# Kernel optimization log

Measured on AMD Instinct MI355X. Metric: run time of the kernel, lower is better.

Reference implementation:

```python
import jax, jax.numpy as jnp
import numpy as np

N, E, DIN, H, D = 100000, 1600000, 256, 4, 32  # nodes, edges, in_feats, heads, out_feats
NEG_SLOPE = 0.2


def setup_inputs() -> dict:
    key = jax.random.key(0)
    ks = jax.random.split(key, 6)
    feat = jax.random.normal(ks[0], (N, DIN), jnp.float32)
    src = jax.random.randint(ks[1], (E,), 0, N, jnp.int32)
    dst = jax.random.randint(ks[2], (E,), 0, N, jnp.int32)
    # fc weight, xavier-normal-ish scale
    W = jax.random.normal(ks[3], (H * D, DIN), jnp.float32) * (2.0 / (DIN + H * D)) ** 0.5
    attn_l = jax.random.normal(ks[4], (1, H, D), jnp.float32) * 0.1
    attn_r = jax.random.normal(ks[5], (1, H, D), jnp.float32) * 0.1
    bias = jnp.zeros((H * D,), jnp.float32)
    return dict(feat=feat, src=src, dst=dst, W=W, attn_l=attn_l, attn_r=attn_r, bias=bias)


def reference(feat, src, dst, W, attn_l, attn_r, bias):
    n = feat.shape[0]
    # node projection: [N, H, D]
    ft = (feat @ W.T).reshape(n, H, D)
    # per-node attention logits: [N, H]
    el = jnp.sum(ft * attn_l, axis=-1)
    er = jnp.sum(ft * attn_r, axis=-1)
    # edge scores (u_add_v + LeakyReLU): [E, H]
    e = jax.nn.leaky_relu(el[src] + er[dst], NEG_SLOPE)
    # segment softmax over incoming edges of each dst node
    m = jax.ops.segment_max(e, dst, num_segments=n)
    m = jnp.where(jnp.isfinite(m), m, 0.0)  # guard zero-in-degree nodes
    ae = jnp.exp(e - m[dst])
    denom = jax.ops.segment_sum(ae, dst, num_segments=n)
    a = ae / denom[dst]  # [E, H]
    # weighted scatter-aggregate (u_mul_e + sum): [N, H, D]
    out = jax.ops.segment_sum(ft[src] * a[:, :, None], dst, num_segments=n)
    return out + bias.reshape(1, H, D)
```

## Files before the change

kernel.cpp:

```cpp
#include <hip/hip_runtime.h>
#include <hip/hip_bf16.h>


#define DIN 256
#define HD 128
#define NEG_SLOPE 0.2f
#define BUCKW 1024
#define BINE 4096
#define CAP  18432

typedef float f32x4 __attribute__((ext_vector_type(4)));
typedef short s16x8 __attribute__((ext_vector_type(8)));

static __device__ __forceinline__ unsigned short f2bf(float x) {
    unsigned u = __float_as_uint(x);
    unsigned r = (u + 0x7FFFu + ((u >> 16) & 1u)) >> 16;
    return (unsigned short)r;
}

__global__ __launch_bounds__(512) void transw_kernel(
    const float* __restrict__ W, unsigned short* __restrict__ Wtb)
{
    int idx = blockIdx.x * blockDim.x + threadIdx.x;
    if (idx >= HD * DIN) return;
    int i = idx & 7, c = (idx >> 3) & 127, kb = idx >> 10;
    Wtb[idx] = f2bf(W[(size_t)c * DIN + kb * 8 + i]);
}

__global__ __launch_bounds__(512, 4) void gemm_bin_kernel(
    const float* __restrict__ feat, const unsigned short* __restrict__ Wtb,
    unsigned short* __restrict__ ftu, const float* __restrict__ attn_l,
    const float* __restrict__ attn_r, float* __restrict__ el,
    float* __restrict__ er, int n,
    const int* __restrict__ src, const int* __restrict__ dst,
    int* __restrict__ gcur, int* __restrict__ esrc,
    unsigned short* __restrict__ edlo, int e, int ngb)
{
    __shared__ int h[128], lb[128], gb[128], sc[128];
    __shared__ int tot;
    __shared__ int ps[BINE];
    __shared__ unsigned short pd[BINE];
    __shared__ unsigned char pb[BINE];
    const int tid = threadIdx.x;

    if ((int)blockIdx.x >= ngb) {
        if (tid < 128) h[tid] = 0;
        __syncthreads();
        const int base = ((int)blockIdx.x - ngb) * BINE + tid * 8;
        int sv[8], dv[8], rk[8];
        const int cnt = min(8, max(0, e - base));
        if (cnt == 8) {
            *(int4*)&sv[0] = *(const int4*)&src[base];
            *(int4*)&sv[4] = *(const int4*)&src[base + 4];
            *(int4*)&dv[0] = *(const int4*)&dst[base];
            *(int4*)&dv[4] = *(const int4*)&dst[base + 4];
        } else {
            for (int m = 0; m < cnt; ++m) { sv[m] = src[base + m]; dv[m] = dst[base + m]; }
        }
        for (int m = 0; m < cnt; ++m)
            rk[m] = atomicAdd(&h[dv[m] >> 10], 1);
        __syncthreads();
        if (tid < 128) sc[tid] = h[tid];
        __syncthreads();
        for (int off = 1; off < 128; off <<= 1) {
            int v = (tid < 128 && tid >= off) ? sc[tid - off] : 0;
            __syncthreads();
            if (tid < 128) sc[tid] += v;
            __syncthreads();
        }
        if (tid < 128) {
            lb[tid] = sc[tid] - h[tid];
            if (h[tid] > 0) gb[tid] = atomicAdd(&gcur[tid], h[tid]);
        }
        if (tid == 127) tot = sc[127];
        __syncthreads();
        for (int m = 0; m < cnt; ++m) {
            int b = dv[m] >> 10;
            int pos = lb[b] + rk[m];
            ps[pos] = sv[m];
            pd[pos] = (unsigned short)(dv[m] & 1023);
            pb[pos] = (unsigned char)b;
        }
        __syncthreads();
        for (int s = tid; s < tot; s += 512) {
            int b = pb[s];
            int o = b * CAP + gb[b] + (s - lb[b]);
            esrc[o] = ps[s];
            edlo[o] = pd[s];
        }
        return;
    }

    const int lane = tid & 63;
    const int wv = tid >> 6;
    const int l16 = lane & 15, lq = lane >> 4;
    const int row0 = (int)blockIdx.x * 128 + wv * 16;
    const int arow = row0 + l16;
    const bool ok = arow < n;
    const float* fp = feat + (size_t)arow * DIN;

    f32x4 acc[8] = {};
#pragma unroll
    for (int kc = 0; kc < 4; ++kc) {
#pragma unroll
        for (int kk = 0; kk < 2; ++kk) {
            const int koff = kc * 64 + kk * 32 + lq * 8;
            union { s16x8 v; __hip_bfloat16 bh[8]; } a;
            a.v = (s16x8)(short)0;
            if (ok) {
                float4 fa = *(const float4*)(fp + koff);
                float4 fb = *(const float4*)(fp + koff + 4);
                a.bh[0] = __float2bfloat16(fa.x);
                a.bh[1] = __float2bfloat16(fa.y);
                a.bh[2] = __float2bfloat16(fa.z);
                a.bh[3] = __float2bfloat16(fa.w);
                a.bh[4] = __float2bfloat16(fb.x);
                a.bh[5] = __float2bfloat16(fb.y);
                a.bh[6] = __float2bfloat16(fb.z);
                a.bh[7] = __float2bfloat16(fb.w);
            }
            const int kb = kc * 8 + kk * 4 + lq;
            const unsigned short* bp = Wtb + ((size_t)kb * 128 + l16) * 8;
#pragma unroll
            for (int n4 = 0; n4 < 8; ++n4) {
                s16x8 b = *(const s16x8*)(bp + n4 * 128);
                acc[n4] = __builtin_amdgcn_mfma_f32_16x16x32_bf16(a.v, b, acc[n4], 0, 0, 0);
            }
        }
    }

    float al8[8], ar8[8];
#pragma unroll
    for (int n4 = 0; n4 < 8; ++n4) {
        al8[n4] = attn_l[n4 * 16 + l16];
        ar8[n4] = attn_r[n4 * 16 + l16];
    }
#pragma unroll
    for (int n4 = 0; n4 < 8; ++n4)
#pragma unroll
        for (int j = 0; j < 4; ++j) {
            int r = row0 + lq * 4 + j;
            if (r < n) ftu[(size_t)r * HD + n4 * 16 + l16] = f2bf(acc[n4][j]);
        }
#pragma unroll
    for (int j = 0; j < 4; ++j) {
        const int r = row0 + lq * 4 + j;
#pragma unroll
        for (int hh = 0; hh < 4; ++hh) {
            float sl = acc[2 * hh][j] * al8[2 * hh] + acc[2 * hh + 1][j] * al8[2 * hh + 1];
            float sr = acc[2 * hh][j] * ar8[2 * hh] + acc[2 * hh + 1][j] * ar8[2 * hh + 1];
#pragma unroll
            for (int off = 1; off < 16; off <<= 1) {
                sl += __shfl_xor(sl, off);
                sr += __shfl_xor(sr, off);
            }
            if (l16 == ((j << 2) | hh) && r < n) {
                el[r * 4 + hh] = sl;
                er[r * 4 + hh] = sr;
            }
        }
    }
}

__global__ __launch_bounds__(1024) void fine_kernel(
    const int* __restrict__ esrc, const unsigned short* __restrict__ edlo,
    const int* __restrict__ gcur, int* __restrict__ beg, int* __restrict__ endp,
    int* __restrict__ srcs_sorted, int n)
{
    __shared__ int deg[1024];
    __shared__ int wsum[16];
    const int b = blockIdx.x, tid = threadIdx.x;
    const int lane = tid & 63, wid = tid >> 6;
    const int lo = b * CAP;
    const int cnt = gcur[b];
    const int nbase = b << 10;
    deg[tid] = 0;
    __syncthreads();
    for (int i = tid; i < cnt; i += 1024)
        atomicAdd(&deg[edlo[lo + i]], 1);
    __syncthreads();
    const int d = deg[tid];
    int x = d;
#pragma unroll
    for (int off = 1; off < 64; off <<= 1) {
        int y = __shfl(x, lane - off);
        if (lane >= off) x += y;
    }
    if (lane == 63) wsum[wid] = x;
    __syncthreads();
    if (tid == 0) {
        int run = 0;
#pragma unroll
        for (int i2 = 0; i2 < 16; ++i2) { int t2 = wsum[i2]; wsum[i2] = run; run += t2; }
    }
    __syncthreads();
    const int start = lo + wsum[wid] + x - d;
    if (nbase + tid < n) {
        beg[nbase + tid] = start;
        endp[nbase + tid] = start + d;
    }
    deg[tid] = start;
    __syncthreads();
    for (int i = tid; i < cnt; i += 1024) {
        int dd = edlo[lo + i];
        int pos = atomicAdd(&deg[dd], 1);
        srcs_sorted[pos] = esrc[lo + i];
    }
}

__global__ __launch_bounds__(256) void aggregate_kernel(
    const unsigned short* __restrict__ ftu, const float* __restrict__ el,
    const float* __restrict__ er, const int* __restrict__ beg,
    const int* __restrict__ endp, const int* __restrict__ srcs,
    const float* __restrict__ bias, float* __restrict__ out, int n)
{
    __shared__ float plds[4][64][4];
    int v = (int)((blockIdx.x * (unsigned)blockDim.x + threadIdx.x) >> 6);
    if (v >= n) return;
    const int wv = (threadIdx.x >> 6) & 3;
    const int lane = threadIdx.x & 63;
    const int h = lane >> 4;
    const int beg_ = beg[v], end_ = endp[v];
    const float4 er4 = *(const float4*)(er + (size_t)v * 4);
    const uint* __restrict__ ftu32 = (const uint*)ftu;
    float* pl = &plds[wv][0][0];
    float dn = 0.f;
    float acc0 = 0.f, acc1 = 0.f;
    for (int t = beg_; t < end_; t += 64) {
        const int cnt = min(64, end_ - t);
        int sj = 0;
        float p0 = 0.f, p1 = 0.f, p2 = 0.f, p3 = 0.f;
        if (lane < cnt) {
            sj = srcs[t + lane];
            float4 elv = *(const float4*)(el + (size_t)sj * 4);
            float e0 = elv.x + er4.x, e1 = elv.y + er4.y;
            float e2 = elv.z + er4.z, e3 = elv.w + er4.w;
            e0 = fmaxf(e0, NEG_SLOPE * e0);
            e1 = fmaxf(e1, NEG_SLOPE * e1);
            e2 = fmaxf(e2, NEG_SLOPE * e2);
            e3 = fmaxf(e3, NEG_SLOPE * e3);
            p0 = __expf(e0); p1 = __expf(e1);
            p2 = __expf(e2); p3 = __expf(e3);
        }
        *(float4*)&pl[lane << 2] = make_float4(p0, p1, p2, p3);
        __builtin_amdgcn_wave_barrier();
        for (int j = 0; j < cnt; j += 16) {
            uint u[16];
            float pj[16];
#pragma unroll
            for (int m = 0; m < 16; ++m) {
                int sjb = __shfl(sj, j + m);
                u[m] = ftu32[(uint)sjb * 64u + (uint)lane];
                pj[m] = pl[((j + m) << 2) + h];
            }
#pragma unroll
            for (int m = 0; m < 16; ++m) {
                dn += pj[m];
                acc0 = fmaf(pj[m], __uint_as_float(u[m] << 16), acc0);
                acc1 = fmaf(pj[m], __uint_as_float(u[m] & 0xffff0000u), acc1);
            }
        }
        __builtin_amdgcn_wave_barrier();
    }
    float inv = dn > 0.f ? 1.f / dn : 0.f;
    float b0 = bias[lane << 1], b1 = bias[(lane << 1) + 1];
    float2 o = make_float2(fmaf(acc0, inv, b0), fmaf(acc1, inv, b1));
    *(float2*)&out[(size_t)v * HD + (lane << 1)] = o;
}

extern "C" void kernel_launch(void* const* d_in, const int* in_sizes, int n_in,
                              void* d_out, int out_size, void* d_ws, size_t ws_size,
                              hipStream_t stream) {
    const float* feat   = (const float*)d_in[0];
    const int*   src    = (const int*)d_in[1];
    const int*   dst    = (const int*)d_in[2];
    const float* W      = (const float*)d_in[3];
    const float* attn_l = (const float*)d_in[4];
    const float* attn_r = (const float*)d_in[5];
    const float* bias   = (const float*)d_in[6];
    float* out = (float*)d_out;
    const int N = in_sizes[0] / DIN;
    const int E = in_sizes[1];
    const int NBUCK = (N + BUCKW - 1) / BUCKW;
    const int NGB = (N + 127) / 128;
    const int EB = (E + BINE - 1) / BINE;

    char* w = (char*)d_ws;
    auto alloc = [&](size_t bytes) {
        char* p = w;
        w += (bytes + 255) & ~(size_t)255;
        return p;
    };
    unsigned short* Wtb         = (unsigned short*)alloc((size_t)DIN * HD * 2);
    unsigned short* ftu         = (unsigned short*)alloc((size_t)N * HD * 2);
    float*          el          = (float*)alloc((size_t)N * 4 * 4);
    float*          er          = (float*)alloc((size_t)N * 4 * 4);
    int*            beg         = (int*)alloc((size_t)N * 4);
    int*            endp        = (int*)alloc((size_t)N * 4);
    int*            srcs_sorted = (int*)alloc((size_t)NBUCK * CAP * 4);
    int*            esrc        = (int*)alloc((size_t)NBUCK * CAP * 4);
    unsigned short* edlo        = (unsigned short*)alloc((size_t)NBUCK * CAP * 2);
    int*            gcur        = (int*)alloc(128 * 4);
    (void)ws_size;

    hipMemsetAsync(gcur, 0, 128 * 4, stream);
    transw_kernel<<<(HD * DIN + 511) / 512, 512, 0, stream>>>(W, Wtb);
    gemm_bin_kernel<<<NGB + EB, 512, 0, stream>>>(
        feat, Wtb, ftu, attn_l, attn_r, el, er, N,
        src, dst, gcur, esrc, edlo, E, NGB);
    fine_kernel<<<NBUCK, 1024, 0, stream>>>(esrc, edlo, gcur, beg, endp, srcs_sorted, N);
    aggregate_kernel<<<(N + 3) / 4, 256, 0, stream>>>(
        ftu, el, er, beg, endp, srcs_sorted, bias, out, N);
}
```

Measured before the change: 158.8 us.

## Regroup kernels: fuse weight transpose with binning, GEMM with fine sort

Moves the weight transpose into block 0 of the edge-binning kernel and fuses the per-bucket fine counting sort into the GEMM launch as extra blocks. This cuts one kernel launch and lets the fine sort overlap with the projection GEMM. The GEMM now stages a 64-row bf16 tile of the features in XOR-swizzled LDS with 256-thread blocks, instead of converting rows straight into registers. The fine sort runs with 256 threads, each handling 4 nodes, so each block has less parallelism. The single transpose block now sits on the critical path before the GEMM.

```diff
diff --git a/kernel.cpp b/kernel.cpp
--- a/kernel.cpp
+++ b/kernel.cpp
@@ -18,23 +18,11 @@
     return (unsigned short)r;
 }
 
-__global__ __launch_bounds__(512) void transw_kernel(
-    const float* __restrict__ W, unsigned short* __restrict__ Wtb)
-{
-    int idx = blockIdx.x * blockDim.x + threadIdx.x;
-    if (idx >= HD * DIN) return;
-    int i = idx & 7, c = (idx >> 3) & 127, kb = idx >> 10;
-    Wtb[idx] = f2bf(W[(size_t)c * DIN + kb * 8 + i]);
-}
-
-__global__ __launch_bounds__(512, 4) void gemm_bin_kernel(
-    const float* __restrict__ feat, const unsigned short* __restrict__ Wtb,
-    unsigned short* __restrict__ ftu, const float* __restrict__ attn_l,
-    const float* __restrict__ attn_r, float* __restrict__ el,
-    float* __restrict__ er, int n,
+__global__ __launch_bounds__(512) void transw_bin_kernel(
+    const float* __restrict__ W, unsigned short* __restrict__ Wtb,
     const int* __restrict__ src, const int* __restrict__ dst,
     int* __restrict__ gcur, int* __restrict__ esrc,
-    unsigned short* __restrict__ edlo, int e, int ngb)
+    unsigned short* __restrict__ edlo, int e)
 {
     __shared__ int h[128], lb[128], gb[128], sc[128];
     __shared__ int tot;
@@ -43,50 +31,121 @@
     __shared__ unsigned char pb[BINE];
     const int tid = threadIdx.x;
 
+    if (blockIdx.x == 0) {
+        for (int idx = tid; idx < HD * DIN; idx += 512) {
+            int i = idx & 7, c = (idx >> 3) & 127, kb = idx >> 10;
+            Wtb[idx] = f2bf(W[(size_t)c * DIN + kb * 8 + i]);
+        }
+        return;
+    }
+
+    if (tid < 128) h[tid] = 0;
+    __syncthreads();
+    const int base = ((int)blockIdx.x - 1) * BINE + tid * 8;
+    int sv[8], dv[8], rk[8];
+    const int cnt = min(8, max(0, e - base));
+    if (cnt == 8) {
+        *(int4*)&sv[0] = *(const int4*)&src[base];
+        *(int4*)&sv[4] = *(const int4*)&src[base + 4];
+        *(int4*)&dv[0] = *(const int4*)&dst[base];
+        *(int4*)&dv[4] = *(const int4*)&dst[base + 4];
+    } else {
+        for (int m = 0; m < cnt; ++m) { sv[m] = src[base + m]; dv[m] = dst[base + m]; }
+    }
+    for (int m = 0; m < cnt; ++m)
+        rk[m] = atomicAdd(&h[dv[m] >> 10], 1);
+    __syncthreads();
+    if (tid < 128) sc[tid] = h[tid];
+    __syncthreads();
+    for (int off = 1; off < 128; off <<= 1) {
+        int v = (tid < 128 && tid >= off) ? sc[tid - off] : 0;
+        __syncthreads();
+        if (tid < 128) sc[tid] += v;
+        __syncthreads();
+    }
+    if (tid < 128) {
+        lb[tid] = sc[tid] - h[tid];
+        if (h[tid] > 0) gb[tid] = atomicAdd(&gcur[tid], h[tid]);
+    }
+    if (tid == 127) tot = sc[127];
+    __syncthreads();
+    for (int m = 0; m < cnt; ++m) {
+        int b = dv[m] >> 10;
+        int pos = lb[b] + rk[m];
+        ps[pos] = sv[m];
+        pd[pos] = (unsigned short)(dv[m] & 1023);
+        pb[pos] = (unsigned char)b;
+    }
+    __syncthreads();
+    for (int s = tid; s < tot; s += 512) {
+        int b = pb[s];
+        int o = b * CAP + gb[b] + (s - lb[b]);
+        esrc[o] = ps[s];
+        edlo[o] = pd[s];
+    }
+}
+
+__global__ __launch_bounds__(256, 5) void gemm_fine_kernel(
+    const float* __restrict__ feat, const unsigned short* __restrict__ Wtb,
+    unsigned short* __restrict__ ftu, const float* __restrict__ attn_l,
+    const float* __restrict__ attn_r, float* __restrict__ el,
+    float* __restrict__ er, int n,
+    const int* __restrict__ esrc, const unsigned short* __restrict__ edlo,
+    const int* __restrict__ gcur, int* __restrict__ beg, int* __restrict__ endp,
+    int* __restrict__ srcs_sorted, int ngb)
+{
+    __shared__ unsigned short As[16384];
+    const int tid = threadIdx.x;
+
     if ((int)blockIdx.x >= ngb) {
-        if (tid < 128) h[tid] = 0;
-        __syncthreads();
-        const int base = ((int)blockIdx.x - ngb) * BINE + tid * 8;
-        int sv[8], dv[8], rk[8];
-        const int cnt = min(8, max(0, e - base));
-        if (cnt == 8) {
-            *(int4*)&sv[0] = *(const int4*)&src[base];
-            *(int4*)&sv[4] = *(const int4*)&src[base + 4];
-            *(int4*)&dv[0] = *(const int4*)&dst[base];
-            *(int4*)&dv[4] = *(const int4*)&dst[base + 4];
+        int* deg = (int*)As;
+        int* wsum = (int*)As + 1024;
+        const int b = (int)blockIdx.x - ngb;
+        const int lane = tid & 63, wid = tid >> 6;
+        const int lo = b * CAP;
+        const int cnt = gcur[b];
+        const int nbase = b << 10;
+        *(int4*)&deg[tid * 4] = make_int4(0, 0, 0, 0);
+        __syncthreads();
+        for (int i = tid; i < cnt; i += 256)
+            atomicAdd(&deg[edlo[lo + i]], 1);
+        __syncthreads();
+        const int4 d4 = *(const int4*)&deg[tid * 4];
+        const int s = d4.x + d4.y + d4.z + d4.w;
+        int x = s;
+#pragma unroll
+        for (int off = 1; off < 64; off <<= 1) {
+            int y = __shfl(x, lane - off);
+            if (lane >= off) x += y;
+        }
+        if (lane == 63) wsum[wid] = x;
+        __syncthreads();
+        if (tid == 0) {
+            int run = 0;
+#pragma unroll
+            for (int i2 = 0; i2 < 4; ++i2) { int t2 = wsum[i2]; wsum[i2] = run; run += t2; }
+        }
+        __syncthreads();
+        const int st0 = lo + wsum[wid] + x - s;
+        const int st1 = st0 + d4.x, st2 = st1 + d4.y, st3 = st2 + d4.z;
+        const int nd = nbase + tid * 4;
+        if (nd + 3 < n) {
+            *(int4*)&beg[nd]  = make_int4(st0, st1, st2, st3);
+            *(int4*)&endp[nd] = make_int4(st0 + d4.x, st1 + d4.y, st2 + d4.z, st3 + d4.w);
         } else {
-            for (int m = 0; m < cnt; ++m) { sv[m] = src[base + m]; dv[m] = dst[base + m]; }
-        }
-        for (int m = 0; m < cnt; ++m)
-            rk[m] = atomicAdd(&h[dv[m] >> 10], 1);
-        __syncthreads();
-        if (tid < 128) sc[tid] = h[tid];
-        __syncthreads();
-        for (int off = 1; off < 128; off <<= 1) {
-            int v = (tid < 128 && tid >= off) ? sc[tid - off] : 0;
-            __syncthreads();
-            if (tid < 128) sc[tid] += v;
-            __syncthreads();
-        }
-        if (tid < 128) {
-            lb[tid] = sc[tid] - h[tid];
-            if (h[tid] > 0) gb[tid] = atomicAdd(&gcur[tid], h[tid]);
-        }
-        if (tid == 127) tot = sc[127];
-        __syncthreads();
-        for (int m = 0; m < cnt; ++m) {
-            int b = dv[m] >> 10;
-            int pos = lb[b] + rk[m];
-            ps[pos] = sv[m];
-            pd[pos] = (unsigned short)(dv[m] & 1023);
-            pb[pos] = (unsigned char)b;
-        }
-        __syncthreads();
-        for (int s = tid; s < tot; s += 512) {
-            int b = pb[s];
-            int o = b * CAP + gb[b] + (s - lb[b]);
-            esrc[o] = ps[s];
-            edlo[o] = pd[s];
+            const int dd[4] = {d4.x, d4.y, d4.z, d4.w};
+            const int ss[4] = {st0, st1, st2, st3};
+#pragma unroll
+            for (int i2 = 0; i2 < 4; ++i2)
+                if (nd + i2 < n) { beg[nd + i2] = ss[i2]; endp[nd + i2] = ss[i2] + dd[i2]; }
+        }
+        __syncthreads();
+        *(int4*)&deg[tid * 4] = make_int4(st0, st1, st2, st3);
+        __syncthreads();
+        for (int i = tid; i < cnt; i += 256) {
+            int dd = edlo[lo + i];
+            int pos = atomicAdd(&deg[dd], 1);
+            srcs_sorted[pos] = esrc[lo + i];
         }
         return;
     }
@@ -94,38 +153,46 @@
     const int lane = tid & 63;
     const int wv = tid >> 6;
     const int l16 = lane & 15, lq = lane >> 4;
-    const int row0 = (int)blockIdx.x * 128 + wv * 16;
-    const int arow = row0 + l16;
-    const bool ok = arow < n;
-    const float* fp = feat + (size_t)arow * DIN;
+    const int row0 = (int)blockIdx.x * 64 + wv * 16;
+    unsigned short* Aw = As + wv * 4096;
+
+#pragma unroll
+    for (int i = 0; i < 8; ++i) {
+        const int c = i * 64 + lane;
+        const int r = c >> 5, u = c & 31;
+        const int grow = row0 + r;
+        union { uint4 q; __hip_bfloat16 bh[8]; } pk;
+        pk.q = make_uint4(0, 0, 0, 0);
+        if (grow < n) {
+            const float* ap = feat + (size_t)grow * DIN + u * 8;
+            float4 fa = *(const float4*)ap;
+            float4 fb = *(const float4*)(ap + 4);
+            pk.bh[0] = __float2bfloat16(fa.x);
+            pk.bh[1] = __float2bfloat16(fa.y);
+            pk.bh[2] = __float2bfloat16(fa.z);
+            pk.bh[3] = __float2bfloat16(fa.w);
+            pk.bh[4] = __float2bfloat16(fb.x);
+            pk.bh[5] = __float2bfloat16(fb.y);
+            pk.bh[6] = __float2bfloat16(fb.z);
+            pk.bh[7] = __float2bfloat16(fb.w);
+        }
+        const int su = u ^ (r & 7);
+        *(uint4*)&Aw[r * 256 + su * 8] = pk.q;
+    }
+    __syncthreads();
 
     f32x4 acc[8] = {};
 #pragma unroll
-    for (int kc = 0; kc < 4; ++kc) {
-#pragma unroll
-        for (int kk = 0; kk < 2; ++kk) {
-            const int koff = kc * 64 + kk * 32 + lq * 8;
-            union { s16x8 v; __hip_bfloat16 bh[8]; } a;
-            a.v = (s16x8)(short)0;
-            if (ok) {
-                float4 fa = *(const float4*)(fp + koff);
-                float4 fb = *(const float4*)(fp + koff + 4);
-                a.bh[0] = __float2bfloat16(fa.x);
-                a.bh[1] = __float2bfloat16(fa.y);
-                a.bh[2] = __float2bfloat16(fa.z);
-                a.bh[3] = __float2bfloat16(fa.w);
-                a.bh[4] = __float2bfloat16(fb.x);
-                a.bh[5] = __float2bfloat16(fb.y);
-                a.bh[6] = __float2bfloat16(fb.z);
-                a.bh[7] = __float2bfloat16(fb.w);
-            }
-            const int kb = kc * 8 + kk * 4 + lq;
-            const unsigned short* bp = Wtb + ((size_t)kb * 128 + l16) * 8;
-#pragma unroll
-            for (int n4 = 0; n4 < 8; ++n4) {
-                s16x8 b = *(const s16x8*)(bp + n4 * 128);
-                acc[n4] = __builtin_amdgcn_mfma_f32_16x16x32_bf16(a.v, b, acc[n4], 0, 0, 0);
-            }
+    for (int kc = 0; kc < 8; ++kc) {
+        const int u = kc * 4 + lq;
+        const int su = u ^ (l16 & 7);
+        s16x8 a = *(const s16x8*)&Aw[l16 * 256 + su * 8];
+        const int kb = kc * 4 + lq;
+        const unsigned short* bp = Wtb + ((size_t)kb * 128 + l16) * 8;
+#pragma unroll
+        for (int n4 = 0; n4 < 8; ++n4) {
+            s16x8 b = *(const s16x8*)(bp + n4 * 128);
+            acc[n4] = __builtin_amdgcn_mfma_f32_16x16x32_bf16(a, b, acc[n4], 0, 0, 0);
         }
     }
 
@@ -159,52 +226,6 @@
                 er[r * 4 + hh] = sr;
             }
         }
-    }
-}
-
-__global__ __launch_bounds__(1024) void fine_kernel(
-    const int* __restrict__ esrc, const unsigned short* __restrict__ edlo,
-    const int* __restrict__ gcur, int* __restrict__ beg, int* __restrict__ endp,
-    int* __restrict__ srcs_sorted, int n)
-{
-    __shared__ int deg[1024];
-    __shared__ int wsum[16];
-    const int b = blockIdx.x, tid = threadIdx.x;
-    const int lane = tid & 63, wid = tid >> 6;
-    const int lo = b * CAP;
-    const int cnt = gcur[b];
-    const int nbase = b << 10;
-    deg[tid] = 0;
-    __syncthreads();
-    for (int i = tid; i < cnt; i += 1024)
-        atomicAdd(&deg[edlo[lo + i]], 1);
-    __syncthreads();
-    const int d = deg[tid];
-    int x = d;
-#pragma unroll
-    for (int off = 1; off < 64; off <<= 1) {
-        int y = __shfl(x, lane - off);
-        if (lane >= off) x += y;
-    }
-    if (lane == 63) wsum[wid] = x;
-    __syncthreads();
-    if (tid == 0) {
-        int run = 0;
-#pragma unroll
-        for (int i2 = 0; i2 < 16; ++i2) { int t2 = wsum[i2]; wsum[i2] = run; run += t2; }
-    }
-    __syncthreads();
-    const int start = lo + wsum[wid] + x - d;
-    if (nbase + tid < n) {
-        beg[nbase + tid] = start;
-        endp[nbase + tid] = start + d;
-    }
-    deg[tid] = start;
-    __syncthreads();
-    for (int i = tid; i < cnt; i += 1024) {
-        int dd = edlo[lo + i];
-        int pos = atomicAdd(&deg[dd], 1);
-        srcs_sorted[pos] = esrc[lo + i];
     }
 }
 
@@ -282,7 +303,7 @@
     const int N = in_sizes[0] / DIN;
     const int E = in_sizes[1];
     const int NBUCK = (N + BUCKW - 1) / BUCKW;
-    const int NGB = (N + 127) / 128;
+    const int NGB = (N + 63) / 64;
     const int EB = (E + BINE - 1) / BINE;
 
     char* w = (char*)d_ws;
@@ -304,11 +325,10 @@
     (void)ws_size;
 
     hipMemsetAsync(gcur, 0, 128 * 4, stream);
-    transw_kernel<<<(HD * DIN + 511) / 512, 512, 0, stream>>>(W, Wtb);
-    gemm_bin_kernel<<<NGB + EB, 512, 0, stream>>>(
+    transw_bin_kernel<<<1 + EB, 512, 0, stream>>>(W, Wtb, src, dst, gcur, esrc, edlo, E);
+    gemm_fine_kernel<<<NGB + NBUCK, 256, 0, stream>>>(
         feat, Wtb, ftu, attn_l, attn_r, el, er, N,
-        src, dst, gcur, esrc, edlo, E, NGB);
-    fine_kernel<<<NBUCK, 1024, 0, stream>>>(esrc, edlo, gcur, beg, endp, srcs_sorted, N);
+        esrc, edlo, gcur, beg, endp, srcs_sorted, NGB);
     aggregate_kernel<<<(N + 3) / 4, 256, 0, stream>>>(
         ftu, el, er, beg, endp, srcs_sorted, bias, out, N);
 }
```

Measured after the change: 187.7 us. 18.2% more time.
